# Kernel tuning notes

Measured on AMD Instinct MI355X. Metric: run time of the kernel, lower is better.

## Reference

```python
import jax, jax.numpy as jnp
import numpy as np
import math

# ---- static config (mirrors init_kwargs) ----
B, CIN, COUT = 8, 32, 32
H, W = 256, 256
RADIUS_CUTOFF = 0.03
NR, NPHI = 6, 7               # kernel_shape = [6, 7] (anisotropic basis)
K = (NR - 1) * NPHI + 1       # 36 basis functions
EPS = 1e-5                    # InstanceNorm2d eps
NEG_SLOPE = 0.2


def _disco_psi(nh, nw, r_cutoff, nr, nphi):
    """Local DISCO filter basis on an equidistant [-1,1]^2 grid.
    Returns psi [K, P, P] (float32) and half-width p (P = 2p+1).
    Piecewise-linear hat functions in radius (nr rings incl. center) times
    hat functions in angle (nphi sectors), normalized and quadrature-weighted."""
    dy = 2.0 / nh
    dx = 2.0 / nw
    p = int(math.floor(r_cutoff / min(dx, dy)))
    off_y = (np.arange(-p, p + 1) * dy)[:, None]
    off_x = (np.arange(-p, p + 1) * dx)[None, :]
    r = np.sqrt(off_x ** 2 + off_y ** 2)                 # [P, P]
    phi = np.arctan2(off_y + 0 * off_x, off_x + 0 * off_y) % (2.0 * np.pi)
    dr = r_cutoff / nr
    dphi = 2.0 * np.pi / nphi
    ker = (nr - 1) * nphi + 1
    ik = np.arange(ker)[:, None, None]                   # [K,1,1]
    ir = ((ik - 1) // nphi + 1) * dr                     # ik=0 -> ring at r=0
    iphi = ((ik - 1) % nphi) * dphi
    norm = np.pi * (r_cutoff * nr / (nr + 1)) ** 2       # 2d normalization
    rv = np.clip(1.0 - np.abs(r[None] - ir) / dr, 0.0, None) * (r[None] <= r_cutoff)
    dphi_abs = np.abs(phi[None] - iphi)
    dphi_min = np.minimum(dphi_abs, 2.0 * np.pi - dphi_abs)
    pv = np.where(ik > 0, np.clip(1.0 - dphi_min / dphi, 0.0, None), 1.0)
    q = dx * dy                                          # quadrature weight
    psi = (rv * pv) * (q / norm)
    return jnp.asarray(psi, jnp.float32), p


def _upsample2x_bilinear_align_corners(x):
    """torch nn.Upsample(scale_factor=2, mode='bilinear', align_corners=True)."""
    b, c, hi, wi = x.shape
    ho, wo = 2 * hi, 2 * wi
    ys = jnp.linspace(0.0, hi - 1.0, ho)
    y0 = jnp.clip(jnp.floor(ys), 0, hi - 2).astype(jnp.int32)
    wy = (ys - y0.astype(ys.dtype))[None, None, :, None]
    x = x[:, :, y0, :] * (1.0 - wy) + x[:, :, y0 + 1, :] * wy
    xs = jnp.linspace(0.0, wi - 1.0, wo)
    x0 = jnp.clip(jnp.floor(xs), 0, wi - 2).astype(jnp.int32)
    wx = (xs - x0.astype(xs.dtype))[None, None, None, :]
    return x[:, :, :, x0] * (1.0 - wx) + x[:, :, :, x0 + 1] * wx


def setup_inputs() -> dict:
    key = jax.random.key(0)
    k1, k2 = jax.random.split(key)
    image = jax.random.normal(k1, (B, CIN, H, W), dtype=jnp.float32)
    # DISCO learnable weights: [out_ch, in_ch, kernel_size]
    scale = 1.0 / np.sqrt(CIN * K)
    weight = jax.random.normal(k2, (COUT, CIN, K), dtype=jnp.float32) * scale
    return {"image": image, "weight": weight}


def reference(image, weight):
    x = _upsample2x_bilinear_align_corners(image)
    # 2) equidistant DISCO conv: assemble dense kernel from basis, strided conv back to (H,W)
    psi, p = _disco_psi(2 * H, 2 * W, RADIUS_CUTOFF / 2.0, NR, NPHI)   # [K,P,P]
    kernel = jnp.einsum("oik,kyx->oiyx", weight, psi)                   # [O,I,P,P]
    y = jax.lax.conv_general_dilated(
        x, kernel, window_strides=(2, 2), padding=[(p, p), (p, p)],
        dimension_numbers=("NCHW", "OIHW", "NCHW"))                     # [B,O,H,W]
    # 3) InstanceNorm2d (no affine), biased variance over spatial dims
    mean = jnp.mean(y, axis=(2, 3), keepdims=True)
    var = jnp.var(y, axis=(2, 3), keepdims=True)
    y = (y - mean) * jax.lax.rsqrt(var + EPS)
    # 4) LeakyReLU(0.2)
    return jnp.where(y >= 0, y, NEG_SLOPE * y)
```

## Files before the change

### kernel.cpp

```cpp
#include <hip/hip_runtime.h>
#include <hip/hip_bf16.h>
#include <math.h>

#define B_     8
#define CIN_   32
#define COUT_  32
#define H_     256
#define W_     256
#define K_     36
#define P_     3
#define KW_    7
#define TAPS_  49
#define EPS_   1e-5f
#define SLOPE_ 0.2f

#define PART_OFF_F  25600

#define IMG_PLANE_B   6736
#define IMG_ROW_B     336

using short8_t  = __attribute__((ext_vector_type(8)))  short;
using f32x16_t  = __attribute__((ext_vector_type(16))) float;
using f32x4_t   = __attribute__((ext_vector_type(4)))  float;

#define SWZ(a) ((a) ^ ((((a) >> 7) & 1) << 4))

__device__ inline ushort f32_to_bf16(float f) {
    unsigned int bits = __float_as_uint(f);
    unsigned int r = (bits + 0x7FFFu + ((bits >> 16) & 1u)) >> 16;
    return (ushort)r;
}

__global__ __launch_bounds__(256)
void build_kernel(const float* __restrict__ weight, ushort* __restrict__ kerB) {
    __shared__ float psi_s[K_];
    const int tap = blockIdx.x;
    const int ty  = tap / KW_;
    const int tx  = tap % KW_;
    const int tid = threadIdx.x;

    if (tid < K_) {
        const double dxy   = 2.0 / 512.0;
        const double rcut  = 0.015;
        const int    nr    = 6, nphi = 7;
        const double dr    = rcut / nr;
        const double dphi  = 2.0 * M_PI / nphi;
        const double norm  = M_PI * (rcut * nr / (nr + 1)) * (rcut * nr / (nr + 1));
        const double q     = dxy * dxy;

        const double offy = (double)(ty - P_) * dxy;
        const double offx = (double)(tx - P_) * dxy;
        const double r    = sqrt(offx * offx + offy * offy);
        double phi = atan2(offy, offx);
        if (phi < 0.0) phi += 2.0 * M_PI;

        const int k = tid;
        double ir, iphi;
        if (k == 0) { ir = 0.0; iphi = 0.0; }
        else        { ir = (double)((k - 1) / nphi + 1) * dr;
                      iphi = (double)((k - 1) % nphi) * dphi; }

        double rv = 1.0 - fabs(r - ir) / dr;
        rv = rv > 0.0 ? rv : 0.0;
        if (r > rcut) rv = 0.0;

        double pv = 1.0;
        if (k > 0) {
            double da = fabs(phi - iphi);
            double dm = da < (2.0 * M_PI - da) ? da : (2.0 * M_PI - da);
            pv = 1.0 - dm / dphi;
            pv = pv > 0.0 ? pv : 0.0;
        }
        psi_s[k] = (float)(rv * pv * q / norm);
    }
    __syncthreads();

    for (int e = tid; e < 1024; e += 256) {
        const int g16  = e >> 9;
        const int lane = (e >> 3) & 63;
        const int j    = e & 7;
        const int o    = lane & 31;
        const int ci   = g16 * 16 + ((lane >> 5) & 1) * 8 + j;
        const float* w = weight + (size_t)(o * CIN_ + ci) * K_;
        float s = 0.f;
        #pragma unroll
        for (int k = 0; k < K_; ++k) s = fmaf(w[k], psi_s[k], s);
        kerB[((size_t)(g16 * 49 + tap) * 64 + lane) * 8 + j] = f32_to_bf16(s);
    }
}

__global__ __launch_bounds__(512, 4)
void conv_mfma(const float* __restrict__ image,
               const ushort* __restrict__ kerB,
               float* __restrict__ out,
               float* __restrict__ partials) {
    __shared__ float  Img_s[6736];
    __shared__ ushort Xup_s[2738 * 8];
    __shared__ float  wp[8][32][2];

    const int tid  = threadIdx.x;
    const int lane = tid & 63;
    const int w    = tid >> 6;
    const int j0 = blockIdx.x * 16;
    const int i0 = blockIdx.y * 16;
    const int b  = blockIdx.z;

    const int u0 = 2 * i0 - 3;
    const int v0 = 2 * j0 - 3;
    const int R0 = i0 - 2;
    const int C0 = j0 - 2;

    const int gs  = lane >> 5;
    const int tio = (lane & 31) >> 4;
    const int tj  = lane & 15;
    const int yb0 = 4 * w + 2 * tio;
    const int xb  = 2 * tj;

    f32x16_t acc;
    #pragma unroll
    for (int q = 0; q < 16; ++q) acc[q] = 0.f;

    char* img_bytes = (char*)Img_s;
    char* xup_bytes = (char*)Xup_s;

    for (int g16 = 0; g16 < 2; ++g16) {
        const float* img = image + (size_t)(b * CIN_ + g16 * 16) * (H_ * W_);
        for (int e = tid; e < 1600; e += 512) {
            const int p  = e / 400;
            const int yx = e - p * 400;
            const int py = yx / 20, px = yx - py * 20;
            const int row = R0 + py, col = C0 + px;
            f32x4_t g = {0.f, 0.f, 0.f, 0.f};
            if ((unsigned)row < 256u && (unsigned)col < 256u) {
                const float* q = img + (size_t)p * 4 * (H_ * W_) + row * W_ + col;
                g[0] = q[0];
                g[1] = q[H_ * W_];
                g[2] = q[2 * H_ * W_];
                g[3] = q[3 * H_ * W_];
            }
            *(f32x4_t*)(img_bytes + p * IMG_PLANE_B + (py * 21 + px) * 16) = g;
        }
        __syncthreads();

        for (int e = tid; e < 1406; e += 512) {
            const int g   = (e >= 703) ? 1 : 0;
            const int r   = e - 703 * g;
            const int y   = r / 19;
            const int xp  = r - 19 * y;
            const int x   = 2 * xp;
            const int ry  = y >> 1;
            const float wy =
                (float)((((y & 1) ? 510 : 255)) - (R0 + ry)) * (1.0f / 511.0f);
            const int Ax = C0 + xp;
            const float wx0 = (float)(255 - Ax) * (1.0f / 511.0f);
            const float wx1 = (float)(510 - Ax) * (1.0f / 511.0f);
            const bool oky = ((unsigned)(u0 + y) < 512u);
            const bool ok0 = oky && ((unsigned)(v0 + x) < 512u);
            const bool ok1 = oky && ((unsigned)(v0 + x + 1) < 512u);

            const char* lo = img_bytes + (2 * g) * IMG_PLANE_B
                           + (ry * 21 + xp) * 16;
            const char* hi = lo + IMG_PLANE_B;
            const f32x4_t a00 = *(const f32x4_t*)(lo);
            const f32x4_t a01 = *(const f32x4_t*)(lo + 16);
            const f32x4_t a10 = *(const f32x4_t*)(lo + IMG_ROW_B);
            const f32x4_t a11 = *(const f32x4_t*)(lo + IMG_ROW_B + 16);
            const f32x4_t b00 = *(const f32x4_t*)(hi);
            const f32x4_t b01 = *(const f32x4_t*)(hi + 16);
            const f32x4_t b10 = *(const f32x4_t*)(hi + IMG_ROW_B);
            const f32x4_t b11 = *(const f32x4_t*)(hi + IMG_ROW_B + 16);

            const f32x4_t cA0 = a00 + wy * (a10 - a00);
            const f32x4_t cA1 = a01 + wy * (a11 - a01);
            const f32x4_t cB0 = b00 + wy * (b10 - b00);
            const f32x4_t cB1 = b01 + wy * (b11 - b01);

            const int idx = g * 1369 + y * 37 + x;

            {
                const f32x4_t va = cA0 + wx0 * (cA1 - cA0);
                const f32x4_t vb = cB0 + wx0 * (cB1 - cB0);
                __hip_bfloat162 h0 = __float22bfloat162_rn(make_float2(va[0], va[1]));
                __hip_bfloat162 h1 = __float22bfloat162_rn(make_float2(va[2], va[3]));
                __hip_bfloat162 h2 = __float22bfloat162_rn(make_float2(vb[0], vb[1]));
                __hip_bfloat162 h3 = __float22bfloat162_rn(make_float2(vb[2], vb[3]));
                union { short8_t s8; uint4 u4; } pk;
                pk.u4.x = ok0 ? *(unsigned int*)&h0 : 0u;
                pk.u4.y = ok0 ? *(unsigned int*)&h1 : 0u;
                pk.u4.z = ok0 ? *(unsigned int*)&h2 : 0u;
                pk.u4.w = ok0 ? *(unsigned int*)&h3 : 0u;
                *(short8_t*)(xup_bytes + SWZ(idx << 4)) = pk.s8;
            }
            if (x + 1 < 37) {
                const f32x4_t va = cA0 + wx1 * (cA1 - cA0);
                const f32x4_t vb = cB0 + wx1 * (cB1 - cB0);
                __hip_bfloat162 h0 = __float22bfloat162_rn(make_float2(va[0], va[1]));
                __hip_bfloat162 h1 = __float22bfloat162_rn(make_float2(va[2], va[3]));
                __hip_bfloat162 h2 = __float22bfloat162_rn(make_float2(vb[0], vb[1]));
                __hip_bfloat162 h3 = __float22bfloat162_rn(make_float2(vb[2], vb[3]));
                union { short8_t s8; uint4 u4; } pk;
                pk.u4.x = ok1 ? *(unsigned int*)&h0 : 0u;
                pk.u4.y = ok1 ? *(unsigned int*)&h1 : 0u;
                pk.u4.z = ok1 ? *(unsigned int*)&h2 : 0u;
                pk.u4.w = ok1 ? *(unsigned int*)&h3 : 0u;
                *(short8_t*)(xup_bytes + SWZ((idx + 1) << 4)) = pk.s8;
            }
        }
        __syncthreads();

        const ushort* kbp = kerB + ((size_t)(g16 * 49 * 64 + lane)) * 8;
        #pragma unroll
        for (int ky = 0; ky < KW_; ++ky) {
            short8_t bf[KW_];
            #pragma unroll
            for (int kx = 0; kx < KW_; ++kx)
                bf[kx] = *(const short8_t*)(kbp + (size_t)(ky * KW_ + kx) * 512);
            const int rowbase = (gs * 1369 + (yb0 + ky) * 37 + xb) << 4;
            #pragma unroll
            for (int kx = 0; kx < KW_; ++kx) {
                const int a0 = SWZ(rowbase + (kx << 4));
                const short8_t afrag = *(const short8_t*)(xup_bytes + a0);
                acc = __builtin_amdgcn_mfma_f32_32x32x16_bf16(afrag, bf[kx], acc, 0, 0, 0);
            }
        }
        __syncthreads();
    }

    const int n = lane & 31;
    float* op = out + (size_t)(b * COUT_ + n) * (H_ * W_);
    const int ibase = i0 + 2 * w;
    #pragma unroll
    for (int grp = 0; grp < 4; ++grp) {
        const int ti  = ibase + (grp >> 1);
        const int tjj = j0 + ((grp & 1) ? 8 : 0) + 4 * gs;
        f32x4_t s;
        s[0] = acc[grp * 4 + 0]; s[1] = acc[grp * 4 + 1];
        s[2] = acc[grp * 4 + 2]; s[3] = acc[grp * 4 + 3];
        *(f32x4_t*)(op + (size_t)ti * W_ + tjj) = s;
    }

    float s1 = 0.f, s2 = 0.f;
    #pragma unroll
    for (int q = 0; q < 16; ++q) { s1 += acc[q]; s2 = fmaf(acc[q], acc[q], s2); }
    s1 += __shfl_xor(s1, 32);
    s2 += __shfl_xor(s2, 32);
    if (lane < 32) { wp[w][lane][0] = s1; wp[w][lane][1] = s2; }
    __syncthreads();
    if (tid < 32) {
        float t1 = 0.f, t2 = 0.f;
        #pragma unroll
        for (int wv = 0; wv < 8; ++wv) { t1 += wp[wv][tid][0]; t2 += wp[wv][tid][1]; }
        const int tile = blockIdx.y * 16 + blockIdx.x;
        float2* pp = (float2*)partials;
        pp[((b * 32 + tid) << 8) | tile] = make_float2(t1, t2);
    }
}

__global__ __launch_bounds__(256)
void norm2_kernel(float* __restrict__ y, const float* __restrict__ partials) {
    __shared__ float r1[256];
    __shared__ float r2[256];
    const int tid = threadIdx.x;
    const int blk = blockIdx.x;
    const int bo  = blk >> 6;
    const float2 p = ((const float2*)partials)[(bo << 8) | tid];
    r1[tid] = p.x; r2[tid] = p.y;
    __syncthreads();
    for (int off = 128; off > 0; off >>= 1) {
        if (tid < off) { r1[tid] += r1[tid + off]; r2[tid] += r2[tid + off]; }
        __syncthreads();
    }
    const float inv = 1.0f / 65536.0f;
    const float m   = r1[0] * inv;
    const float var = r2[0] * inv - m * m;
    const float rs  = 1.0f / sqrtf(var + EPS_);

    const int e = blk * 256 + tid;
    float4 v = ((const float4*)y)[e];
    v.x = (v.x - m) * rs; v.x = v.x >= 0.f ? v.x : SLOPE_ * v.x;
    v.y = (v.y - m) * rs; v.y = v.y >= 0.f ? v.y : SLOPE_ * v.y;
    v.z = (v.z - m) * rs; v.z = v.z >= 0.f ? v.z : SLOPE_ * v.z;
    v.w = (v.w - m) * rs; v.w = v.w >= 0.f ? v.w : SLOPE_ * v.w;
    ((float4*)y)[e] = v;
}

extern "C" void kernel_launch(void* const* d_in, const int* in_sizes, int n_in,
                              void* d_out, int out_size, void* d_ws, size_t ws_size,
                              hipStream_t stream) {
    const float* image  = (const float*)d_in[0];
    const float* weight = (const float*)d_in[1];
    float*  out      = (float*)d_out;
    ushort* kerB     = (ushort*)d_ws;
    float*  partials = (float*)d_ws + PART_OFF_F;

    build_kernel<<<dim3(TAPS_), dim3(256), 0, stream>>>(weight, kerB);
    conv_mfma<<<dim3(16, 16, B_), dim3(512), 0, stream>>>(image, kerB, out, partials);
    norm2_kernel<<<dim3(16384), dim3(256), 0, stream>>>(out, partials);
}
```

Measured before the change: 127.6 us.

## Prefetch second channel group into registers during MFMA and split LDS into even/odd planes

```diff
diff --git a/kernel.cpp b/kernel.cpp
--- a/kernel.cpp
+++ b/kernel.cpp
@@ -19,11 +19,15 @@
 #define IMG_PLANE_B   6736
 #define IMG_ROW_B     336
 
+#define E_ROW   304
+#define E_OCT   11248
+#define O_ROW   288
+#define O_OCT   10656
+#define O_BASE  22496
+
 using short8_t  = __attribute__((ext_vector_type(8)))  short;
 using f32x16_t  = __attribute__((ext_vector_type(16))) float;
 using f32x4_t   = __attribute__((ext_vector_type(4)))  float;
-
-#define SWZ(a) ((a) ^ ((((a) >> 7) & 1) << 4))
 
 __device__ inline ushort f32_to_bf16(float f) {
     unsigned int bits = __float_as_uint(f);
@@ -114,7 +118,6 @@
     const int tio = (lane & 31) >> 4;
     const int tj  = lane & 15;
     const int yb0 = 4 * w + 2 * tio;
-    const int xb  = 2 * tj;
 
     f32x16_t acc;
     #pragma unroll
@@ -123,25 +126,32 @@
     char* img_bytes = (char*)Img_s;
     char* xup_bytes = (char*)Xup_s;
 
-    for (int g16 = 0; g16 < 2; ++g16) {
-        const float* img = image + (size_t)(b * CIN_ + g16 * 16) * (H_ * W_);
-        for (int e = tid; e < 1600; e += 512) {
-            const int p  = e / 400;
-            const int yx = e - p * 400;
-            const int py = yx / 20, px = yx - py * 20;
-            const int row = R0 + py, col = C0 + px;
-            f32x4_t g = {0.f, 0.f, 0.f, 0.f};
-            if ((unsigned)row < 256u && (unsigned)col < 256u) {
-                const float* q = img + (size_t)p * 4 * (H_ * W_) + row * W_ + col;
-                g[0] = q[0];
-                g[1] = q[H_ * W_];
-                g[2] = q[2 * H_ * W_];
-                g[3] = q[3 * H_ * W_];
-            }
-            *(f32x4_t*)(img_bytes + p * IMG_PLANE_B + (py * 21 + px) * 16) = g;
+    const float* img0 = image + (size_t)(b * CIN_)       * (H_ * W_);
+    const float* img1 = image + (size_t)(b * CIN_ + 16)  * (H_ * W_);
+
+    auto s1_load = [&](const float* img, int e) -> f32x4_t {
+        const int p  = e / 400;
+        const int yx = e - p * 400;
+        const int py = yx / 20, px = yx - py * 20;
+        const int row = R0 + py, col = C0 + px;
+        f32x4_t g = {0.f, 0.f, 0.f, 0.f};
+        if ((unsigned)row < 256u && (unsigned)col < 256u) {
+            const float* q = img + (size_t)p * 4 * (H_ * W_) + row * W_ + col;
+            g[0] = q[0];
+            g[1] = q[H_ * W_];
+            g[2] = q[2 * (H_ * W_)];
+            g[3] = q[3 * (H_ * W_)];
         }
-        __syncthreads();
-
+        return g;
+    };
+    auto s1_store = [&](int e, f32x4_t g) {
+        const int p  = e / 400;
+        const int yx = e - p * 400;
+        const int py = yx / 20, px = yx - py * 20;
+        *(f32x4_t*)(img_bytes + p * IMG_PLANE_B + (py * 21 + px) * 16) = g;
+    };
+
+    auto stage2 = [&]() {
         for (int e = tid; e < 1406; e += 512) {
             const int g   = (e >= 703) ? 1 : 0;
             const int r   = e - 703 * g;
@@ -175,8 +185,6 @@
             const f32x4_t cB0 = b00 + wy * (b10 - b00);
             const f32x4_t cB1 = b01 + wy * (b11 - b01);
 
-            const int idx = g * 1369 + y * 37 + x;
-
             {
                 const f32x4_t va = cA0 + wx0 * (cA1 - cA0);
                 const f32x4_t vb = cB0 + wx0 * (cB1 - cB0);
@@ -189,9 +197,9 @@
                 pk.u4.y = ok0 ? *(unsigned int*)&h1 : 0u;
                 pk.u4.z = ok0 ? *(unsigned int*)&h2 : 0u;
                 pk.u4.w = ok0 ? *(unsigned int*)&h3 : 0u;
-                *(short8_t*)(xup_bytes + SWZ(idx << 4)) = pk.s8;
+                *(short8_t*)(xup_bytes + g * E_OCT + y * E_ROW + xp * 16) = pk.s8;
             }
-            if (x + 1 < 37) {
+            if (xp < 18) {
                 const f32x4_t va = cA0 + wx1 * (cA1 - cA0);
                 const f32x4_t vb = cB0 + wx1 * (cB1 - cB0);
                 __hip_bfloat162 h0 = __float22bfloat162_rn(make_float2(va[0], va[1]));
@@ -203,28 +211,59 @@
                 pk.u4.y = ok1 ? *(unsigned int*)&h1 : 0u;
                 pk.u4.z = ok1 ? *(unsigned int*)&h2 : 0u;
                 pk.u4.w = ok1 ? *(unsigned int*)&h3 : 0u;
-                *(short8_t*)(xup_bytes + SWZ((idx + 1) << 4)) = pk.s8;
+                *(short8_t*)(xup_bytes + O_BASE + g * O_OCT + y * O_ROW + xp * 16) = pk.s8;
             }
         }
-        __syncthreads();
-
-        const ushort* kbp = kerB + ((size_t)(g16 * 49 * 64 + lane)) * 8;
+    };
+
+    const int ebase = gs * E_OCT + tj * 16;
+    const int obase = O_BASE + gs * O_OCT + tj * 16;
+    auto stage3 = [&](const ushort* kbp) {
         #pragma unroll
         for (int ky = 0; ky < KW_; ++ky) {
             short8_t bf[KW_];
             #pragma unroll
             for (int kx = 0; kx < KW_; ++kx)
                 bf[kx] = *(const short8_t*)(kbp + (size_t)(ky * KW_ + kx) * 512);
-            const int rowbase = (gs * 1369 + (yb0 + ky) * 37 + xb) << 4;
+            const int re = ebase + (yb0 + ky) * E_ROW;
+            const int ro = obase + (yb0 + ky) * O_ROW;
             #pragma unroll
             for (int kx = 0; kx < KW_; ++kx) {
-                const int a0 = SWZ(rowbase + (kx << 4));
-                const short8_t afrag = *(const short8_t*)(xup_bytes + a0);
+                const int addr = ((kx & 1) ? ro : re) + (kx >> 1) * 16;
+                const short8_t afrag = *(const short8_t*)(xup_bytes + addr);
                 acc = __builtin_amdgcn_mfma_f32_32x32x16_bf16(afrag, bf[kx], acc, 0, 0, 0);
             }
         }
-        __syncthreads();
-    }
+    };
+
+    s1_store(tid,        s1_load(img0, tid));
+    s1_store(tid + 512,  s1_load(img0, tid + 512));
+    s1_store(tid + 1024, s1_load(img0, tid + 1024));
+    if (tid < 64) s1_store(tid + 1536, s1_load(img0, tid + 1536));
+    __syncthreads();
+
+    stage2();
+    __syncthreads();
+
+    f32x4_t pf0 = s1_load(img1, tid);
+    f32x4_t pf1 = s1_load(img1, tid + 512);
+    f32x4_t pf2 = s1_load(img1, tid + 1024);
+    f32x4_t pf3 = {0.f, 0.f, 0.f, 0.f};
+    if (tid < 64) pf3 = s1_load(img1, tid + 1536);
+
+    stage3(kerB + (size_t)lane * 8);
+    __syncthreads();
+
+    s1_store(tid,        pf0);
+    s1_store(tid + 512,  pf1);
+    s1_store(tid + 1024, pf2);
+    if (tid < 64) s1_store(tid + 1536, pf3);
+    __syncthreads();
+
+    stage2();
+    __syncthreads();
+
+    stage3(kerB + (size_t)(49 * 64 + lane) * 8);
 
     const int n = lane & 31;
     float* op = out + (size_t)(b * COUT_ + n) * (H_ * W_);
```

New measurement: 131.8 us. +3.3%, slower.

## Pack kx-tap pairs into MFMA K dimension with even/odd column planes

Applied to the files above, without the earlier changes.

```diff
diff --git a/kernel.cpp b/kernel.cpp
--- a/kernel.cpp
+++ b/kernel.cpp
@@ -14,16 +14,17 @@
 #define EPS_   1e-5f
 #define SLOPE_ 0.2f
 
-#define PART_OFF_F  25600
+#define PART_OFF_F  28672
 
 #define IMG_PLANE_B   6736
 #define IMG_ROW_B     336
+
+#define XP_ROW   304
+#define XO_BASE  11248
 
 using short8_t  = __attribute__((ext_vector_type(8)))  short;
 using f32x16_t  = __attribute__((ext_vector_type(16))) float;
 using f32x4_t   = __attribute__((ext_vector_type(4)))  float;
-
-#define SWZ(a) ((a) ^ ((((a) >> 7) & 1) << 4))
 
 __device__ inline ushort f32_to_bf16(float f) {
     unsigned int bits = __float_as_uint(f);
@@ -33,69 +34,75 @@
 
 __global__ __launch_bounds__(256)
 void build_kernel(const float* __restrict__ weight, ushort* __restrict__ kerB) {
-    __shared__ float psi_s[K_];
-    const int tap = blockIdx.x;
-    const int ty  = tap / KW_;
-    const int tx  = tap % KW_;
+    __shared__ float psi_s[2][K_];
+    const int f  = blockIdx.x;
+    const int p  = f & 3;
+    const int ky = (f >> 2) % 7;
+    const int oc = f / 28;
     const int tid = threadIdx.x;
 
-    if (tid < K_) {
-        const double dxy   = 2.0 / 512.0;
-        const double rcut  = 0.015;
-        const int    nr    = 6, nphi = 7;
-        const double dr    = rcut / nr;
-        const double dphi  = 2.0 * M_PI / nphi;
-        const double norm  = M_PI * (rcut * nr / (nr + 1)) * (rcut * nr / (nr + 1));
-        const double q     = dxy * dxy;
-
-        const double offy = (double)(ty - P_) * dxy;
-        const double offx = (double)(tx - P_) * dxy;
-        const double r    = sqrt(offx * offx + offy * offy);
-        double phi = atan2(offy, offx);
-        if (phi < 0.0) phi += 2.0 * M_PI;
-
-        const int k = tid;
-        double ir, iphi;
-        if (k == 0) { ir = 0.0; iphi = 0.0; }
-        else        { ir = (double)((k - 1) / nphi + 1) * dr;
-                      iphi = (double)((k - 1) % nphi) * dphi; }
-
-        double rv = 1.0 - fabs(r - ir) / dr;
-        rv = rv > 0.0 ? rv : 0.0;
-        if (r > rcut) rv = 0.0;
-
-        double pv = 1.0;
-        if (k > 0) {
-            double da = fabs(phi - iphi);
-            double dm = da < (2.0 * M_PI - da) ? da : (2.0 * M_PI - da);
-            pv = 1.0 - dm / dphi;
-            pv = pv > 0.0 ? pv : 0.0;
-        }
-        psi_s[k] = (float)(rv * pv * q / norm);
+    if (tid < 2 * K_) {
+        const int tt = tid / K_;
+        const int k  = tid - tt * K_;
+        const int kx = 2 * p + tt;
+        float val = 0.f;
+        if (kx <= 6) {
+            const double dxy   = 2.0 / 512.0;
+            const double rcut  = 0.015;
+            const int    nr    = 6, nphi = 7;
+            const double dr    = rcut / nr;
+            const double dphi  = 2.0 * M_PI / nphi;
+            const double norm  = M_PI * (rcut * nr / (nr + 1)) * (rcut * nr / (nr + 1));
+            const double q     = dxy * dxy;
+            const double offy = (double)(ky - P_) * dxy;
+            const double offx = (double)(kx - P_) * dxy;
+            const double r    = sqrt(offx * offx + offy * offy);
+            double phi = atan2(offy, offx);
+            if (phi < 0.0) phi += 2.0 * M_PI;
+            double ir, iphi;
+            if (k == 0) { ir = 0.0; iphi = 0.0; }
+            else        { ir = (double)((k - 1) / nphi + 1) * dr;
+                          iphi = (double)((k - 1) % nphi) * dphi; }
+            double rv = 1.0 - fabs(r - ir) / dr;
+            rv = rv > 0.0 ? rv : 0.0;
+            if (r > rcut) rv = 0.0;
+            double pv = 1.0;
+            if (k > 0) {
+                double da = fabs(phi - iphi);
+                double dm = da < (2.0 * M_PI - da) ? da : (2.0 * M_PI - da);
+                pv = 1.0 - dm / dphi;
+                pv = pv > 0.0 ? pv : 0.0;
+            }
+            val = (float)(rv * pv * q / norm);
+        }
+        psi_s[tt][k] = val;
     }
     __syncthreads();
 
-    for (int e = tid; e < 1024; e += 256) {
-        const int g16  = e >> 9;
-        const int lane = (e >> 3) & 63;
+    for (int e = tid; e < 512; e += 256) {
+        const int lane = e >> 3;
         const int j    = e & 7;
-        const int o    = lane & 31;
-        const int ci   = g16 * 16 + ((lane >> 5) & 1) * 8 + j;
-        const float* w = weight + (size_t)(o * CIN_ + ci) * K_;
+        const int gs   = lane >> 5;
+        const int n    = lane & 31;
+        const int kx   = 2 * p + gs;
         float s = 0.f;
-        #pragma unroll
-        for (int k = 0; k < K_; ++k) s = fmaf(w[k], psi_s[k], s);
-        kerB[((size_t)(g16 * 49 + tap) * 64 + lane) * 8 + j] = f32_to_bf16(s);
-    }
-}
-
-__global__ __launch_bounds__(512, 4)
+        if (kx <= 6) {
+            const int ci = oc * 8 + j;
+            const float* w = weight + (size_t)(n * CIN_ + ci) * K_;
+            #pragma unroll
+            for (int k = 0; k < K_; ++k) s = fmaf(w[k], psi_s[gs][k], s);
+        }
+        kerB[((size_t)f * 64 + lane) * 8 + j] = f32_to_bf16(s);
+    }
+}
+
+__global__ __launch_bounds__(512, 8)
 void conv_mfma(const float* __restrict__ image,
                const ushort* __restrict__ kerB,
                float* __restrict__ out,
                float* __restrict__ partials) {
-    __shared__ float  Img_s[6736];
-    __shared__ ushort Xup_s[2738 * 8];
+    __shared__ float  Img_s[3368];
+    __shared__ ushort Xup_s[11248];
     __shared__ float  wp[8][32][2];
 
     const int tid  = threadIdx.x;
@@ -114,7 +121,6 @@
     const int tio = (lane & 31) >> 4;
     const int tj  = lane & 15;
     const int yb0 = 4 * w + 2 * tio;
-    const int xb  = 2 * tj;
 
     f32x16_t acc;
     #pragma unroll
@@ -123,10 +129,12 @@
     char* img_bytes = (char*)Img_s;
     char* xup_bytes = (char*)Xup_s;
 
-    for (int g16 = 0; g16 < 2; ++g16) {
-        const float* img = image + (size_t)(b * CIN_ + g16 * 16) * (H_ * W_);
-        for (int e = tid; e < 1600; e += 512) {
-            const int p  = e / 400;
+    const float* imgb = image + (size_t)(b * CIN_) * (H_ * W_);
+
+    for (int oc = 0; oc < 4; ++oc) {
+        const float* img = imgb + (size_t)(oc * 8) * (H_ * W_);
+        for (int e = tid; e < 800; e += 512) {
+            const int p  = (e >= 400) ? 1 : 0;
             const int yx = e - p * 400;
             const int py = yx / 20, px = yx - py * 20;
             const int row = R0 + py, col = C0 + px;
@@ -135,18 +143,16 @@
                 const float* q = img + (size_t)p * 4 * (H_ * W_) + row * W_ + col;
                 g[0] = q[0];
                 g[1] = q[H_ * W_];
-                g[2] = q[2 * H_ * W_];
-                g[3] = q[3 * H_ * W_];
+                g[2] = q[2 * (H_ * W_)];
+                g[3] = q[3 * (H_ * W_)];
             }
             *(f32x4_t*)(img_bytes + p * IMG_PLANE_B + (py * 21 + px) * 16) = g;
         }
         __syncthreads();
 
-        for (int e = tid; e < 1406; e += 512) {
-            const int g   = (e >= 703) ? 1 : 0;
-            const int r   = e - 703 * g;
-            const int y   = r / 19;
-            const int xp  = r - 19 * y;
+        for (int e = tid; e < 703; e += 512) {
+            const int y   = e / 19;
+            const int xp  = e - 19 * y;
             const int x   = 2 * xp;
             const int ry  = y >> 1;
             const float wy =
@@ -156,10 +162,9 @@
             const float wx1 = (float)(510 - Ax) * (1.0f / 511.0f);
             const bool oky = ((unsigned)(u0 + y) < 512u);
             const bool ok0 = oky && ((unsigned)(v0 + x) < 512u);
-            const bool ok1 = oky && ((unsigned)(v0 + x + 1) < 512u);
-
-            const char* lo = img_bytes + (2 * g) * IMG_PLANE_B
-                           + (ry * 21 + xp) * 16;
+            const bool ok1 = oky && ((unsigned)(v0 + x + 1) < 512u) && (xp < 18);
+
+            const char* lo = img_bytes + (ry * 21 + xp) * 16;
             const char* hi = lo + IMG_PLANE_B;
             const f32x4_t a00 = *(const f32x4_t*)(lo);
             const f32x4_t a01 = *(const f32x4_t*)(lo + 16);
@@ -174,8 +179,6 @@
             const f32x4_t cA1 = a01 + wy * (a11 - a01);
             const f32x4_t cB0 = b00 + wy * (b10 - b00);
             const f32x4_t cB1 = b01 + wy * (b11 - b01);
-
-            const int idx = g * 1369 + y * 37 + x;
 
             {
                 const f32x4_t va = cA0 + wx0 * (cA1 - cA0);
@@ -189,9 +192,9 @@
                 pk.u4.y = ok0 ? *(unsigned int*)&h1 : 0u;
                 pk.u4.z = ok0 ? *(unsigned int*)&h2 : 0u;
                 pk.u4.w = ok0 ? *(unsigned int*)&h3 : 0u;
-                *(short8_t*)(xup_bytes + SWZ(idx << 4)) = pk.s8;
-            }
-            if (x + 1 < 37) {
+                *(short8_t*)(xup_bytes + y * XP_ROW + xp * 16) = pk.s8;
+            }
+            {
                 const f32x4_t va = cA0 + wx1 * (cA1 - cA0);
                 const f32x4_t vb = cB0 + wx1 * (cB1 - cB0);
                 __hip_bfloat162 h0 = __float22bfloat162_rn(make_float2(va[0], va[1]));
@@ -203,24 +206,24 @@
                 pk.u4.y = ok1 ? *(unsigned int*)&h1 : 0u;
                 pk.u4.z = ok1 ? *(unsigned int*)&h2 : 0u;
                 pk.u4.w = ok1 ? *(unsigned int*)&h3 : 0u;
-                *(short8_t*)(xup_bytes + SWZ((idx + 1) << 4)) = pk.s8;
+                *(short8_t*)(xup_bytes + XO_BASE + y * XP_ROW + xp * 16) = pk.s8;
             }
         }
         __syncthreads();
 
-        const ushort* kbp = kerB + ((size_t)(g16 * 49 * 64 + lane)) * 8;
+        const int pbase = (gs ? XO_BASE : 0) + tj * 16;
+        const ushort* kbp = kerB + ((size_t)(oc * 28) * 64 + lane) * 8;
         #pragma unroll
         for (int ky = 0; ky < KW_; ++ky) {
-            short8_t bf[KW_];
+            short8_t bf[4];
             #pragma unroll
-            for (int kx = 0; kx < KW_; ++kx)
-                bf[kx] = *(const short8_t*)(kbp + (size_t)(ky * KW_ + kx) * 512);
-            const int rowbase = (gs * 1369 + (yb0 + ky) * 37 + xb) << 4;
+            for (int p = 0; p < 4; ++p)
+                bf[p] = *(const short8_t*)(kbp + (size_t)(ky * 4 + p) * 512);
+            const int rbase = pbase + (yb0 + ky) * XP_ROW;
             #pragma unroll
-            for (int kx = 0; kx < KW_; ++kx) {
-                const int a0 = SWZ(rowbase + (kx << 4));
-                const short8_t afrag = *(const short8_t*)(xup_bytes + a0);
-                acc = __builtin_amdgcn_mfma_f32_32x32x16_bf16(afrag, bf[kx], acc, 0, 0, 0);
+            for (int p = 0; p < 4; ++p) {
+                const short8_t afrag = *(const short8_t*)(xup_bytes + rbase + p * 16);
+                acc = __builtin_amdgcn_mfma_f32_32x32x16_bf16(afrag, bf[p], acc, 0, 0, 0);
             }
         }
         __syncthreads();
@@ -293,7 +296,7 @@
     ushort* kerB     = (ushort*)d_ws;
     float*  partials = (float*)d_ws + PART_OFF_F;
 
-    build_kernel<<<dim3(TAPS_), dim3(256), 0, stream>>>(weight, kerB);
+    build_kernel<<<dim3(112), dim3(256), 0, stream>>>(weight, kerB);
     conv_mfma<<<dim3(16, 16, B_), dim3(512), 0, stream>>>(image, kerB, out, partials);
     norm2_kernel<<<dim3(16384), dim3(256), 0, stream>>>(out, partials);
 }
```

Measured after the change: 126.7 us. Within noise of the previous version (-0.7%).
